# Optimization experiments

Measured on AMD Instinct MI355X. Metric: run time of the kernel, lower is better.

## Reference

```python
import jax, jax.numpy as jnp
import numpy as np

K = 20      # knn fan-in (constructor arg)
EPS = 1e-5  # LayerNorm eps (torch default)

def ln(x, g, b):
    m = jnp.mean(x, axis=-1, keepdims=True)
    v = jnp.mean((x - m) ** 2, axis=-1, keepdims=True)
    return (x - m) / jnp.sqrt(v + EPS) * g + b

def setup_inputs():
    key = jax.random.key(0)
    ks = jax.random.split(key, 12)
    N, Cin, Cout, H = 4096, 128, 128, 512
    def w(k, i, o):
        return (jax.random.normal(k, (i, o), jnp.float32) / np.sqrt(i)).astype(jnp.float32)
    return dict(
        x=jax.random.normal(ks[0], (N, Cin), jnp.float32),
        pos=jax.random.normal(ks[1], (N, 3), jnp.float32),
        batch=jnp.zeros((N,), jnp.int32),
        # PointTransformerConv linears (bias=False in PyG)
        W_lin=w(ks[2], Cin, Cout),
        W_src=w(ks[3], Cin, Cout),
        W_dst=w(ks[4], Cin, Cout),
        # pos_nn: Lin(3,H) LN ELU Lin(H,Cout) LN ELU
        pw1=w(ks[5], 3, H), pb1=jnp.zeros((H,), jnp.float32),
        pg1=jnp.ones((H,), jnp.float32), pbt1=jnp.zeros((H,), jnp.float32),
        pw2=w(ks[6], H, Cout), pb2=jnp.zeros((Cout,), jnp.float32),
        pg2=jnp.ones((Cout,), jnp.float32), pbt2=jnp.zeros((Cout,), jnp.float32),
        # attn_nn: Lin(Cout,H) LN ELU Lin(H,Cout) LN ELU
        aw1=w(ks[7], Cout, H), ab1=jnp.zeros((H,), jnp.float32),
        ag1=jnp.ones((H,), jnp.float32), abt1=jnp.zeros((H,), jnp.float32),
        aw2=w(ks[8], H, Cout), ab2=jnp.zeros((Cout,), jnp.float32),
        ag2=jnp.ones((Cout,), jnp.float32), abt2=jnp.zeros((Cout,), jnp.float32),
    )

def knn_idx(pos):
    # single-graph knn (batch is constant zero); returns [N, K+1] neighbor idx
    # with self-loop appended (PointTransformerConv add_self_loops=True).
    N = pos.shape[0]
    sq = jnp.sum(pos * pos, axis=1)
    d2 = sq[:, None] + sq[None, :] - 2.0 * (pos @ pos.T)      # [N, N]
    d2 = d2.at[jnp.arange(N), jnp.arange(N)].set(jnp.inf)      # loop=False
    _, nbr = jax.lax.top_k(-d2, K)                             # [N, K]
    return jnp.concatenate([nbr, jnp.arange(N)[:, None]], axis=1)

def reference(x, pos, batch, W_lin, W_src, W_dst,
              pw1, pb1, pg1, pbt1, pw2, pb2, pg2, pbt2,
              aw1, ab1, ag1, abt1, aw2, ab2, ag2, abt2):
    idx = knn_idx(pos)                      # [N, K+1] source node per edge
    v = x @ W_lin                           # message values
    a_src = x @ W_src
    a_dst = x @ W_dst
    rel = pos[:, None, :] - pos[idx]        # pos_i - pos_j, [N, K+1, 3]
    h = jax.nn.elu(ln(rel @ pw1 + pb1, pg1, pbt1))
    delta = jax.nn.elu(ln(h @ pw2 + pb2, pg2, pbt2))           # [N, K+1, C]
    alpha = a_dst[:, None, :] - a_src[idx] + delta
    h2 = jax.nn.elu(ln(alpha @ aw1 + ab1, ag1, abt1))
    alpha = jax.nn.elu(ln(h2 @ aw2 + ab2, ag2, abt2))
    alpha = jax.nn.softmax(alpha, axis=1)   # softmax over neighbors of i
    return jnp.sum(alpha * (v[idx] + delta), axis=1)           # [N, C]
```

## Files before the change

### kernel.cpp

```cpp
#include <hip/hip_runtime.h>
#include <math.h>

#define NN    4096
#define CIN   128
#define CO    128
#define HD    512
#define KK    20
#define EE    21
#define EDGES (NN * EE)
#define LNEPS 1e-5f

typedef unsigned short u16;
typedef unsigned int   u32;
typedef unsigned long long u64;
typedef __attribute__((ext_vector_type(8))) short bf16x8;
typedef __attribute__((ext_vector_type(8))) short short8v;
typedef __attribute__((ext_vector_type(4))) float f32x4;

#define MFMA16(a,b,c) __builtin_amdgcn_mfma_f32_16x16x32_bf16(a,b,c,0,0,0)

__device__ __forceinline__ u16 f2b(float x) {
    u32 u = __float_as_uint(x);
    u32 r = u + 0x7fffu + ((u >> 16) & 1u);
    return (u16)(r >> 16);
}
__device__ __forceinline__ float b2f(u16 h) {
    return __uint_as_float(((u32)h) << 16);
}

__global__ __launch_bounds__(64) void k_knn(const float* __restrict__ pos,
                                            int* __restrict__ idxg)
{
    int i = blockIdx.x;
    int lane = threadIdx.x;
    float px = pos[3*i], py = pos[3*i+1], pz = pos[3*i+2];
    float bd[KK]; int bi[KK];
#pragma unroll
    for (int s = 0; s < KK; ++s) { bd[s] = INFINITY; bi[s] = 0x7fffffff; }
    for (int j = lane; j < NN; j += 64) {
        float dx = px - pos[3*j], dy = py - pos[3*j+1], dz = pz - pos[3*j+2];
        float d2 = dx*dx + dy*dy + dz*dz;
        if (j != i && d2 < bd[KK-1]) {
            float cd = d2; int ci = j;
#pragma unroll
            for (int s = 0; s < KK; ++s) {
                bool sw = cd < bd[s];
                float td = sw ? bd[s] : cd;  int ti = sw ? bi[s] : ci;
                bd[s] = sw ? cd : bd[s];     bi[s] = sw ? ci : bi[s];
                cd = td; ci = ti;
            }
        }
    }
    for (int r = 0; r < KK; ++r) {
        u64 m = ~0ull;
#pragma unroll
        for (int s = 0; s < KK; ++s) {
            u64 k = ((u64)__float_as_uint(bd[s]) << 32) | (u32)bi[s];
            m = k < m ? k : m;
        }
#pragma unroll
        for (int off = 32; off > 0; off >>= 1) {
            u64 o = __shfl_xor(m, off, 64);
            m = o < m ? o : m;
        }
        if (lane == 0) idxg[i*EE + r] = (int)(u32)m;
#pragma unroll
        for (int s = 0; s < KK; ++s) {
            u64 k = ((u64)__float_as_uint(bd[s]) << 32) | (u32)bi[s];
            if (k == m) bd[s] = INFINITY;
        }
    }
    if (lane == 0) idxg[i*EE + KK] = i;
}

__global__ __launch_bounds__(256) void k_lin3(const float* __restrict__ x,
        const float* __restrict__ Wl, const float* __restrict__ Ws, const float* __restrict__ Wd,
        float* __restrict__ v, float* __restrict__ as_, float* __restrict__ ad)
{
    __shared__ float sx[8][CIN];
    int b = blockIdx.x, t = threadIdx.x;
    int n0 = b * 8;
    for (int q = t; q < 8*CIN; q += 256) sx[q >> 7][q & 127] = x[n0*CIN + q];
    __syncthreads();
    int c = t & 127, g = t >> 7;
    float al[4] = {0,0,0,0}, asr[4] = {0,0,0,0}, adr[4] = {0,0,0,0};
    for (int k = 0; k < CIN; ++k) {
        float wl = Wl[k*CO + c], ws = Ws[k*CO + c], wd = Wd[k*CO + c];
#pragma unroll
        for (int nn2 = 0; nn2 < 4; ++nn2) {
            float xv = sx[g*4 + nn2][k];
            al[nn2]  = fmaf(xv, wl, al[nn2]);
            asr[nn2] = fmaf(xv, ws, asr[nn2]);
            adr[nn2] = fmaf(xv, wd, adr[nn2]);
        }
    }
#pragma unroll
    for (int nn2 = 0; nn2 < 4; ++nn2) {
        int n = n0 + g*4 + nn2;
        v[n*CO + c]   = al[nn2];
        as_[n*CO + c] = asr[nn2];
        ad[n*CO + c]  = adr[nn2];
    }
}

__global__ __launch_bounds__(256) void k_wconv3(
        const float* __restrict__ aw1, const float* __restrict__ aw2,
        const float* __restrict__ pw2,
        u16* __restrict__ awp1, u16* __restrict__ awp2, u16* __restrict__ pwp2)
{
    int gb = blockIdx.x;
    const float* src; u16* dst; int N, kplog, base;
    if (gb < 256)      { src = aw1; dst = awp1; N = HD; kplog = 2; base = 0;   }
    else if (gb < 512) { src = aw2; dst = awp2; N = CO; kplog = 4; base = 256; }
    else               { src = pw2; dst = pwp2; N = CO; kplog = 4; base = 512; }
    int idx = (gb - base)*256 + threadIdx.x;
    int j  = idx & 7;
    int l  = (idx >> 3) & 63;
    int ks = (idx >> 9) & ((1 << kplog) - 1);
    int nt = idx >> (9 + kplog);
    int k = ks*32 + (l >> 4)*8 + j;
    int c = nt*16 + (l & 15);
    dst[idx] = f2b(src[(size_t)k*N + c]);
}

template<int L>
__device__ __forceinline__ void ln_elu_b16(u16* base, int rows, int stride,
        const float* __restrict__ gam, const float* __restrict__ bet)
{
    constexpr int P = L / 64;
    int t = threadIdx.x, lane = t & 63, w = t >> 6;
    float g[P], b[P];
    if constexpr (P >= 4) {
#pragma unroll
        for (int q = 0; q < P; q += 4) {
            *(float4*)&g[q] = *(const float4*)&gam[lane*P + q];
            *(float4*)&b[q] = *(const float4*)&bet[lane*P + q];
        }
    } else {
        *(float2*)&g[0] = *(const float2*)&gam[lane*P];
        *(float2*)&b[0] = *(const float2*)&bet[lane*P];
    }
    for (int e = w; e < rows; e += 4) {
        u16* row = base + e*stride + lane*P;
        u16 raw[P];
        if constexpr (P == 8) {
            *(ushort4*)&raw[0] = *(const ushort4*)&row[0];
            *(ushort4*)&raw[4] = *(const ushort4*)&row[4];
        } else {
            *(ushort2*)&raw[0] = *(const ushort2*)&row[0];
        }
        float vals[P]; float s = 0.f, sq = 0.f;
#pragma unroll
        for (int q = 0; q < P; ++q) {
            float xx = b2f(raw[q]);
            vals[q] = xx; s += xx; sq += xx*xx;
        }
#pragma unroll
        for (int off = 32; off > 0; off >>= 1) {
            s  += __shfl_xor(s,  off, 64);
            sq += __shfl_xor(sq, off, 64);
        }
        float mn = s * (1.0f / L);
        float rstd = rsqrtf(sq * (1.0f / L) - mn*mn + LNEPS);
#pragma unroll
        for (int q = 0; q < P; ++q) {
            float y = (vals[q] - mn) * rstd * g[q] + b[q];
            y = y > 0.f ? y : __expf(y) - 1.f;
            raw[q] = f2b(y);
        }
        if constexpr (P == 8) {
            *(ushort4*)&row[0] = *(const ushort4*)&raw[0];
            *(ushort4*)&row[4] = *(const ushort4*)&raw[4];
        } else {
            *(ushort2*)&row[0] = *(const ushort2*)&raw[0];
        }
    }
}

#define SA_S 136
#define SH_S 520

__global__ __launch_bounds__(256, 3) void k_posnn(
        const float* __restrict__ pos, const int* __restrict__ idxg,
        const float* __restrict__ pw1, const float* __restrict__ pb1,
        const float* __restrict__ pg1, const float* __restrict__ pbt1,
        const u16* __restrict__ pwp2, const float* __restrict__ pb2,
        const float* __restrict__ pg2, const float* __restrict__ pbt2,
        u16* __restrict__ delta)
{
    __shared__ __align__(16) u16 s_h[32*SH_S];
    __shared__ __align__(16) u16 s_d[32*SA_S];
    __shared__ float s_rel[32][3];
    int t = threadIdx.x;
    int e0g = blockIdx.x * 32;
    if (t < 32) {
        int e = e0g + t;
        u32 ii = (u32)e / 21u;
        int j = idxg[e];
        s_rel[t][0] = pos[3*ii]   - pos[3*j];
        s_rel[t][1] = pos[3*ii+1] - pos[3*j+1];
        s_rel[t][2] = pos[3*ii+2] - pos[3*j+2];
    }
    __syncthreads();
    {
        int c1 = t, c2 = t + 256;
        float wa0 = pw1[c1], wa1 = pw1[HD + c1], wa2 = pw1[2*HD + c1], ba = pb1[c1];
        float wb0 = pw1[c2], wb1 = pw1[HD + c2], wb2 = pw1[2*HD + c2], bb = pb1[c2];
        for (int r = 0; r < 32; ++r) {
            float r0 = s_rel[r][0], r1 = s_rel[r][1], r2 = s_rel[r][2];
            s_h[r*SH_S + c1] = f2b(ba + r0*wa0 + r1*wa1 + r2*wa2);
            s_h[r*SH_S + c2] = f2b(bb + r0*wb0 + r1*wb1 + r2*wb2);
        }
    }
    __syncthreads();
    ln_elu_b16<HD>(s_h, 32, SH_S, pg1, pbt1);
    __syncthreads();
    {
        int w = t >> 6, l = t & 63, lr = l & 15, lk = l >> 4;
        int m = w & 1, nt0 = (w >> 1) * 4;
        bf16x8 afr[16];
#pragma unroll
        for (int ks = 0; ks < 16; ++ks)
            afr[ks] = *(const bf16x8*)&s_h[(m*16 + lr)*SH_S + ks*32 + lk*8];
#pragma unroll
        for (int n2 = 0; n2 < 4; ++n2) {
            int nt = nt0 + n2;
            const u16* bp = pwp2 + ((size_t)nt*16*64 + l)*8;
            f32x4 acc = {0.f, 0.f, 0.f, 0.f};
#pragma unroll
            for (int ks = 0; ks < 16; ++ks) {
                bf16x8 bfr = *(const bf16x8*)(bp + ks*512);
                acc = MFMA16(afr[ks], bfr, acc);
            }
            float bias = pb2[nt*16 + lr];
#pragma unroll
            for (int r = 0; r < 4; ++r)
                s_d[(m*16 + lk*4 + r)*SA_S + nt*16 + lr] = f2b(acc[r] + bias);
        }
    }
    __syncthreads();
    ln_elu_b16<CO>(s_d, 32, SA_S, pg2, pbt2);
    __syncthreads();
    {
        int el = t >> 3, c0 = (t & 7) << 4;
        size_t gb = (size_t)(e0g + el)*CO + c0;
        *(short8v*)&delta[gb]     = *(const short8v*)&s_d[el*SA_S + c0];
        *(short8v*)&delta[gb + 8] = *(const short8v*)&s_d[el*SA_S + c0 + 8];
    }
}

__global__ __launch_bounds__(256, 3) void k_amlp(
        const int* __restrict__ idxg,
        const float* __restrict__ as_, const float* __restrict__ ad,
        const u16* __restrict__ delta,
        const u16* __restrict__ awp1, const float* __restrict__ ab1,
        const float* __restrict__ ag1, const float* __restrict__ abt1,
        const u16* __restrict__ awp2, const float* __restrict__ ab2,
        const float* __restrict__ ag2, const float* __restrict__ abt2,
        u16* __restrict__ alphaF)
{
    __shared__ __align__(16) u16 s_a[32*SA_S];
    __shared__ __align__(16) u16 s_h[32*SH_S];
    __shared__ __align__(16) u16 s_af[32*SA_S];
    int t = threadIdx.x;
    int e0g = blockIdx.x * 32;
    {
        int el = t >> 3, c0 = (t & 7) << 4;
        int e = e0g + el;
        int i = (int)((u32)e / 21u);
        int j = idxg[e];
        const float* adp = ad  + i*CIN + c0;
        const float* asp = as_ + j*CIN + c0;
        const u16*  dp   = delta + (size_t)e*CO + c0;
        u16* op = &s_a[el*SA_S + c0];
#pragma unroll
        for (int q = 0; q < 16; q += 8) {
            float4 a0 = *(const float4*)(adp + q);
            float4 a1 = *(const float4*)(adp + q + 4);
            float4 s0 = *(const float4*)(asp + q);
            float4 s1 = *(const float4*)(asp + q + 4);
            short8v d8 = *(const short8v*)(dp + q);
            short8v o;
            o[0] = (short)f2b(a0.x - s0.x + b2f((u16)d8[0]));
            o[1] = (short)f2b(a0.y - s0.y + b2f((u16)d8[1]));
            o[2] = (short)f2b(a0.z - s0.z + b2f((u16)d8[2]));
            o[3] = (short)f2b(a0.w - s0.w + b2f((u16)d8[3]));
            o[4] = (short)f2b(a1.x - s1.x + b2f((u16)d8[4]));
            o[5] = (short)f2b(a1.y - s1.y + b2f((u16)d8[5]));
            o[6] = (short)f2b(a1.z - s1.z + b2f((u16)d8[6]));
            o[7] = (short)f2b(a1.w - s1.w + b2f((u16)d8[7]));
            *(short8v*)(op + q) = o;
        }
    }
    __syncthreads();
    int w = t >> 6, l = t & 63, lr = l & 15, lk = l >> 4;
    {
        int m = w & 1, nt0 = (w >> 1) * 16;
        bf16x8 afr[4];
#pragma unroll
        for (int ks = 0; ks < 4; ++ks)
            afr[ks] = *(const bf16x8*)&s_a[(m*16 + lr)*SA_S + ks*32 + lk*8];
#pragma unroll
        for (int n2 = 0; n2 < 16; ++n2) {
            int nt = nt0 + n2;
            const u16* bp = awp1 + ((size_t)nt*4*64 + l)*8;
            f32x4 acc = {0.f, 0.f, 0.f, 0.f};
#pragma unroll
            for (int ks = 0; ks < 4; ++ks) {
                bf16x8 bfr = *(const bf16x8*)(bp + ks*512);
                acc = MFMA16(afr[ks], bfr, acc);
            }
            float bias = ab1[nt*16 + lr];
#pragma unroll
            for (int r = 0; r < 4; ++r)
                s_h[(m*16 + lk*4 + r)*SH_S + nt*16 + lr] = f2b(acc[r] + bias);
        }
    }
    __syncthreads();
    ln_elu_b16<HD>(s_h, 32, SH_S, ag1, abt1);
    __syncthreads();
    {
        int m = w & 1, nt0 = (w >> 1) * 4;
        bf16x8 afr[16];
#pragma unroll
        for (int ks = 0; ks < 16; ++ks)
            afr[ks] = *(const bf16x8*)&s_h[(m*16 + lr)*SH_S + ks*32 + lk*8];
#pragma unroll
        for (int n2 = 0; n2 < 4; ++n2) {
            int nt = nt0 + n2;
            const u16* bp = awp2 + ((size_t)nt*16*64 + l)*8;
            f32x4 acc = {0.f, 0.f, 0.f, 0.f};
#pragma unroll
            for (int ks = 0; ks < 16; ++ks) {
                bf16x8 bfr = *(const bf16x8*)(bp + ks*512);
                acc = MFMA16(afr[ks], bfr, acc);
            }
            float bias = ab2[nt*16 + lr];
#pragma unroll
            for (int r = 0; r < 4; ++r)
                s_af[(m*16 + lk*4 + r)*SA_S + nt*16 + lr] = f2b(acc[r] + bias);
        }
    }
    __syncthreads();
    ln_elu_b16<CO>(s_af, 32, SA_S, ag2, abt2);
    __syncthreads();
    {
        int el = t >> 3, c0 = (t & 7) << 4;
        size_t gb = (size_t)(e0g + el)*CO + c0;
        *(short8v*)&alphaF[gb]     = *(const short8v*)&s_af[el*SA_S + c0];
        *(short8v*)&alphaF[gb + 8] = *(const short8v*)&s_af[el*SA_S + c0 + 8];
    }
}

__global__ __launch_bounds__(256) void k_agg(
        const int* __restrict__ idxg,
        const float* __restrict__ v, const u16* __restrict__ delta,
        const u16* __restrict__ alphaF, float* __restrict__ out)
{
    __shared__ int s_idx[8][EE];
    int b = blockIdx.x, t = threadIdx.x;
    int n0 = b * 8;
    for (int q = t; q < 8*EE; q += 256) s_idx[q/EE][q%EE] = idxg[n0*EE + q];
    __syncthreads();
    int c = t & 127, g = t >> 7;
    for (int ng = g; ng < 8; ng += 2) {
        int i = n0 + ng;
        size_t base = (size_t)i*EE*CO + c;
        float af[EE]; float mx = -INFINITY;
#pragma unroll
        for (int e = 0; e < EE; ++e) { af[e] = b2f(alphaF[base + e*CO]); mx = fmaxf(mx, af[e]); }
        float ssum = 0.f;
#pragma unroll
        for (int e = 0; e < EE; ++e) { af[e] = __expf(af[e] - mx); ssum += af[e]; }
        float accv = 0.f;
#pragma unroll
        for (int e = 0; e < EE; ++e) {
            int j = s_idx[ng][e];
            float msg = v[j*CO + c] + b2f(delta[base + e*CO]);
            accv = fmaf(af[e], msg, accv);
        }
        out[i*CO + c] = accv / ssum;
    }
}

extern "C" void kernel_launch(void* const* d_in, const int* in_sizes, int n_in,
                              void* d_out, int out_size, void* d_ws, size_t ws_size,
                              hipStream_t stream)
{
    const float* x    = (const float*)d_in[0];
    const float* pos  = (const float*)d_in[1];
    const float* Wl   = (const float*)d_in[3];
    const float* Wsrc = (const float*)d_in[4];
    const float* Wdst = (const float*)d_in[5];
    const float* pw1  = (const float*)d_in[6];
    const float* pb1  = (const float*)d_in[7];
    const float* pg1  = (const float*)d_in[8];
    const float* pbt1 = (const float*)d_in[9];
    const float* pw2  = (const float*)d_in[10];
    const float* pb2  = (const float*)d_in[11];
    const float* pg2  = (const float*)d_in[12];
    const float* pbt2 = (const float*)d_in[13];
    const float* aw1  = (const float*)d_in[14];
    const float* ab1  = (const float*)d_in[15];
    const float* ag1  = (const float*)d_in[16];
    const float* abt1 = (const float*)d_in[17];
    const float* aw2  = (const float*)d_in[18];
    const float* ab2  = (const float*)d_in[19];
    const float* ag2  = (const float*)d_in[20];
    const float* abt2 = (const float*)d_in[21];
    float* out = (float*)d_out;

    char* ws = (char*)d_ws;
    int*   idxg   = (int*)ws;
    u16*   awp1   = (u16*)(ws + 0x54000);
    u16*   awp2   = (u16*)(ws + 0x74000);
    u16*   pwp2   = (u16*)(ws + 0x94000);
    float* v      = (float*)(ws + 0xC0000);
    float* asrc   = (float*)(ws + 0x2C0000);
    float* adst   = (float*)(ws + 0x4C0000);
    u16*   delta  = (u16*)(ws + 0x6C0000);
    u16*   alphaF = (u16*)(ws + 0x6C0000 + 0x1500000);

    k_knn   <<<NN,       64,  0, stream>>>(pos, idxg);
    k_wconv3<<<768,      256, 0, stream>>>(aw1, aw2, pw2, awp1, awp2, pwp2);
    k_lin3  <<<NN/8,     256, 0, stream>>>(x, Wl, Wsrc, Wdst, v, asrc, adst);
    k_posnn <<<EDGES/32, 256, 0, stream>>>(pos, idxg, pw1, pb1, pg1, pbt1,
                                           pwp2, pb2, pg2, pbt2, delta);
    k_amlp  <<<EDGES/32, 256, 0, stream>>>(idxg, asrc, adst, delta,
                                           awp1, ab1, ag1, abt1,
                                           awp2, ab2, ag2, abt2, alphaF);
    k_agg   <<<NN/8,     256, 0, stream>>>(idxg, v, delta, alphaF, out);
}
```

Before: 301.8 us.

## Double block size to 512 threads in edge MLP kernels, keep second GEMM output in fp32

The posnn and attention-MLP kernels now launch 512 threads (8 waves) per 32-edge tile, so each wave computes half as many MFMA output tiles and LayerNorm rows. The second linear's output is kept in fp32 in shared memory, skipping a bf16 round trip before the final LayerNorm, and is converted to bf16 only on the global store. This adds parallelism per tile but raises shared memory use and drops the occupancy hint of 3 blocks, so occupancy may change.

```diff
diff --git a/kernel.cpp b/kernel.cpp
--- a/kernel.cpp
+++ b/kernel.cpp
@@ -14,7 +14,6 @@
 typedef unsigned int   u32;
 typedef unsigned long long u64;
 typedef __attribute__((ext_vector_type(8))) short bf16x8;
-typedef __attribute__((ext_vector_type(8))) short short8v;
 typedef __attribute__((ext_vector_type(4))) float f32x4;
 
 #define MFMA16(a,b,c) __builtin_amdgcn_mfma_f32_16x16x32_bf16(a,b,c,0,0,0)
@@ -123,32 +122,23 @@
     dst[idx] = f2b(src[(size_t)k*N + c]);
 }
 
-template<int L>
+template<int L, int NW>
 __device__ __forceinline__ void ln_elu_b16(u16* base, int rows, int stride,
         const float* __restrict__ gam, const float* __restrict__ bet)
 {
     constexpr int P = L / 64;
     int t = threadIdx.x, lane = t & 63, w = t >> 6;
     float g[P], b[P];
-    if constexpr (P >= 4) {
-#pragma unroll
-        for (int q = 0; q < P; q += 4) {
-            *(float4*)&g[q] = *(const float4*)&gam[lane*P + q];
-            *(float4*)&b[q] = *(const float4*)&bet[lane*P + q];
-        }
-    } else {
-        *(float2*)&g[0] = *(const float2*)&gam[lane*P];
-        *(float2*)&b[0] = *(const float2*)&bet[lane*P];
-    }
-    for (int e = w; e < rows; e += 4) {
+#pragma unroll
+    for (int q = 0; q < P; q += 4) {
+        *(float4*)&g[q] = *(const float4*)&gam[lane*P + q];
+        *(float4*)&b[q] = *(const float4*)&bet[lane*P + q];
+    }
+    for (int e = w; e < rows; e += NW) {
         u16* row = base + e*stride + lane*P;
         u16 raw[P];
-        if constexpr (P == 8) {
-            *(ushort4*)&raw[0] = *(const ushort4*)&row[0];
-            *(ushort4*)&raw[4] = *(const ushort4*)&row[4];
-        } else {
-            *(ushort2*)&raw[0] = *(const ushort2*)&row[0];
-        }
+        *(ushort4*)&raw[0] = *(const ushort4*)&row[0];
+        *(ushort4*)&raw[4] = *(const ushort4*)&row[4];
         float vals[P]; float s = 0.f, sq = 0.f;
 #pragma unroll
         for (int q = 0; q < P; ++q) {
@@ -168,19 +158,48 @@
             y = y > 0.f ? y : __expf(y) - 1.f;
             raw[q] = f2b(y);
         }
-        if constexpr (P == 8) {
-            *(ushort4*)&row[0] = *(const ushort4*)&raw[0];
-            *(ushort4*)&row[4] = *(const ushort4*)&raw[4];
-        } else {
-            *(ushort2*)&row[0] = *(const ushort2*)&raw[0];
-        }
+        *(ushort4*)&row[0] = *(const ushort4*)&raw[0];
+        *(ushort4*)&row[4] = *(const ushort4*)&raw[4];
+    }
+}
+
+template<int L, int NW>
+__device__ __forceinline__ void ln_elu_f32v(float* base, int rows, int stride,
+        const float* __restrict__ gam, const float* __restrict__ bet)
+{
+    constexpr int P = L / 64;
+    int t = threadIdx.x, lane = t & 63, w = t >> 6;
+    float g[P], b[P];
+    *(float2*)&g[0] = *(const float2*)&gam[lane*P];
+    *(float2*)&b[0] = *(const float2*)&bet[lane*P];
+    for (int e = w; e < rows; e += NW) {
+        float* row = base + e*stride + lane*P;
+        float vals[P];
+        *(float2*)&vals[0] = *(const float2*)&row[0];
+        float s = 0.f, sq = 0.f;
+#pragma unroll
+        for (int q = 0; q < P; ++q) { s += vals[q]; sq += vals[q]*vals[q]; }
+#pragma unroll
+        for (int off = 32; off > 0; off >>= 1) {
+            s  += __shfl_xor(s,  off, 64);
+            sq += __shfl_xor(sq, off, 64);
+        }
+        float mn = s * (1.0f / L);
+        float rstd = rsqrtf(sq * (1.0f / L) - mn*mn + LNEPS);
+#pragma unroll
+        for (int q = 0; q < P; ++q) {
+            float y = (vals[q] - mn) * rstd * g[q] + b[q];
+            vals[q] = y > 0.f ? y : __expf(y) - 1.f;
+        }
+        *(float2*)&row[0] = *(const float2*)&vals[0];
     }
 }
 
 #define SA_S 136
 #define SH_S 520
-
-__global__ __launch_bounds__(256, 3) void k_posnn(
+#define SF_S 132
+
+__global__ __launch_bounds__(512) void k_posnn(
         const float* __restrict__ pos, const int* __restrict__ idxg,
         const float* __restrict__ pw1, const float* __restrict__ pb1,
         const float* __restrict__ pg1, const float* __restrict__ pbt1,
@@ -188,8 +207,8 @@
         const float* __restrict__ pg2, const float* __restrict__ pbt2,
         u16* __restrict__ delta)
 {
-    __shared__ __align__(16) u16 s_h[32*SH_S];
-    __shared__ __align__(16) u16 s_d[32*SA_S];
+    __shared__ __align__(16) u16   s_h[32*SH_S];
+    __shared__ __align__(16) float s_d[32*SF_S];
     __shared__ float s_rel[32][3];
     int t = threadIdx.x;
     int e0g = blockIdx.x * 32;
@@ -203,27 +222,25 @@
     }
     __syncthreads();
     {
-        int c1 = t, c2 = t + 256;
+        int c1 = t;
         float wa0 = pw1[c1], wa1 = pw1[HD + c1], wa2 = pw1[2*HD + c1], ba = pb1[c1];
-        float wb0 = pw1[c2], wb1 = pw1[HD + c2], wb2 = pw1[2*HD + c2], bb = pb1[c2];
         for (int r = 0; r < 32; ++r) {
-            float r0 = s_rel[r][0], r1 = s_rel[r][1], r2 = s_rel[r][2];
-            s_h[r*SH_S + c1] = f2b(ba + r0*wa0 + r1*wa1 + r2*wa2);
-            s_h[r*SH_S + c2] = f2b(bb + r0*wb0 + r1*wb1 + r2*wb2);
-        }
-    }
-    __syncthreads();
-    ln_elu_b16<HD>(s_h, 32, SH_S, pg1, pbt1);
+            float hv = fmaf(s_rel[r][2], wa2, fmaf(s_rel[r][1], wa1, fmaf(s_rel[r][0], wa0, ba)));
+            s_h[r*SH_S + c1] = f2b(hv);
+        }
+    }
+    __syncthreads();
+    ln_elu_b16<HD, 8>(s_h, 32, SH_S, pg1, pbt1);
     __syncthreads();
     {
         int w = t >> 6, l = t & 63, lr = l & 15, lk = l >> 4;
-        int m = w & 1, nt0 = (w >> 1) * 4;
+        int m = w & 1, nt0 = (w >> 1) * 2;
         bf16x8 afr[16];
 #pragma unroll
         for (int ks = 0; ks < 16; ++ks)
             afr[ks] = *(const bf16x8*)&s_h[(m*16 + lr)*SH_S + ks*32 + lk*8];
 #pragma unroll
-        for (int n2 = 0; n2 < 4; ++n2) {
+        for (int n2 = 0; n2 < 2; ++n2) {
             int nt = nt0 + n2;
             const u16* bp = pwp2 + ((size_t)nt*16*64 + l)*8;
             f32x4 acc = {0.f, 0.f, 0.f, 0.f};
@@ -235,21 +252,27 @@
             float bias = pb2[nt*16 + lr];
 #pragma unroll
             for (int r = 0; r < 4; ++r)
-                s_d[(m*16 + lk*4 + r)*SA_S + nt*16 + lr] = f2b(acc[r] + bias);
-        }
-    }
-    __syncthreads();
-    ln_elu_b16<CO>(s_d, 32, SA_S, pg2, pbt2);
-    __syncthreads();
-    {
-        int el = t >> 3, c0 = (t & 7) << 4;
-        size_t gb = (size_t)(e0g + el)*CO + c0;
-        *(short8v*)&delta[gb]     = *(const short8v*)&s_d[el*SA_S + c0];
-        *(short8v*)&delta[gb + 8] = *(const short8v*)&s_d[el*SA_S + c0 + 8];
-    }
-}
-
-__global__ __launch_bounds__(256, 3) void k_amlp(
+                s_d[(m*16 + lk*4 + r)*SF_S + nt*16 + lr] = acc[r] + bias;
+        }
+    }
+    __syncthreads();
+    ln_elu_f32v<CO, 8>(s_d, 32, SF_S, pg2, pbt2);
+    __syncthreads();
+    {
+        int el = t >> 4, c0 = (t & 15) << 3;
+        const float* sp = &s_d[el*SF_S + c0];
+        float4 v0 = *(const float4*)(sp);
+        float4 v1 = *(const float4*)(sp + 4);
+        bf16x8 o;
+        o[0] = (short)f2b(v0.x); o[1] = (short)f2b(v0.y);
+        o[2] = (short)f2b(v0.z); o[3] = (short)f2b(v0.w);
+        o[4] = (short)f2b(v1.x); o[5] = (short)f2b(v1.y);
+        o[6] = (short)f2b(v1.z); o[7] = (short)f2b(v1.w);
+        *(bf16x8*)&delta[(size_t)(e0g + el)*CO + c0] = o;
+    }
+}
+
+__global__ __launch_bounds__(512) void k_amlp(
         const int* __restrict__ idxg,
         const float* __restrict__ as_, const float* __restrict__ ad,
         const u16* __restrict__ delta,
@@ -259,49 +282,45 @@
         const float* __restrict__ ag2, const float* __restrict__ abt2,
         u16* __restrict__ alphaF)
 {
-    __shared__ __align__(16) u16 s_a[32*SA_S];
-    __shared__ __align__(16) u16 s_h[32*SH_S];
-    __shared__ __align__(16) u16 s_af[32*SA_S];
+    __shared__ __align__(16) u16   s_a[32*SA_S];
+    __shared__ __align__(16) u16   s_h[32*SH_S];
+    __shared__ __align__(16) float s_af[32*SF_S];
     int t = threadIdx.x;
     int e0g = blockIdx.x * 32;
     {
-        int el = t >> 3, c0 = (t & 7) << 4;
+        int el = t >> 4, c0 = (t & 15) << 3;
         int e = e0g + el;
         int i = (int)((u32)e / 21u);
         int j = idxg[e];
         const float* adp = ad  + i*CIN + c0;
         const float* asp = as_ + j*CIN + c0;
         const u16*  dp   = delta + (size_t)e*CO + c0;
-        u16* op = &s_a[el*SA_S + c0];
-#pragma unroll
-        for (int q = 0; q < 16; q += 8) {
-            float4 a0 = *(const float4*)(adp + q);
-            float4 a1 = *(const float4*)(adp + q + 4);
-            float4 s0 = *(const float4*)(asp + q);
-            float4 s1 = *(const float4*)(asp + q + 4);
-            short8v d8 = *(const short8v*)(dp + q);
-            short8v o;
-            o[0] = (short)f2b(a0.x - s0.x + b2f((u16)d8[0]));
-            o[1] = (short)f2b(a0.y - s0.y + b2f((u16)d8[1]));
-            o[2] = (short)f2b(a0.z - s0.z + b2f((u16)d8[2]));
-            o[3] = (short)f2b(a0.w - s0.w + b2f((u16)d8[3]));
-            o[4] = (short)f2b(a1.x - s1.x + b2f((u16)d8[4]));
-            o[5] = (short)f2b(a1.y - s1.y + b2f((u16)d8[5]));
-            o[6] = (short)f2b(a1.z - s1.z + b2f((u16)d8[6]));
-            o[7] = (short)f2b(a1.w - s1.w + b2f((u16)d8[7]));
-            *(short8v*)(op + q) = o;
-        }
+        float4 a0 = *(const float4*)(adp);
+        float4 a1 = *(const float4*)(adp + 4);
+        float4 s0 = *(const float4*)(asp);
+        float4 s1 = *(const float4*)(asp + 4);
+        bf16x8 d8 = *(const bf16x8*)(dp);
+        bf16x8 o;
+        o[0] = (short)f2b(a0.x - s0.x + b2f((u16)d8[0]));
+        o[1] = (short)f2b(a0.y - s0.y + b2f((u16)d8[1]));
+        o[2] = (short)f2b(a0.z - s0.z + b2f((u16)d8[2]));
+        o[3] = (short)f2b(a0.w - s0.w + b2f((u16)d8[3]));
+        o[4] = (short)f2b(a1.x - s1.x + b2f((u16)d8[4]));
+        o[5] = (short)f2b(a1.y - s1.y + b2f((u16)d8[5]));
+        o[6] = (short)f2b(a1.z - s1.z + b2f((u16)d8[6]));
+        o[7] = (short)f2b(a1.w - s1.w + b2f((u16)d8[7]));
+        *(bf16x8*)&s_a[el*SA_S + c0] = o;
     }
     __syncthreads();
     int w = t >> 6, l = t & 63, lr = l & 15, lk = l >> 4;
     {
-        int m = w & 1, nt0 = (w >> 1) * 16;
+        int m = w & 1, nt0 = (w >> 1) * 8;
         bf16x8 afr[4];
 #pragma unroll
         for (int ks = 0; ks < 4; ++ks)
             afr[ks] = *(const bf16x8*)&s_a[(m*16 + lr)*SA_S + ks*32 + lk*8];
 #pragma unroll
-        for (int n2 = 0; n2 < 16; ++n2) {
+        for (int n2 = 0; n2 < 8; ++n2) {
             int nt = nt0 + n2;
             const u16* bp = awp1 + ((size_t)nt*4*64 + l)*8;
             f32x4 acc = {0.f, 0.f, 0.f, 0.f};
@@ -317,16 +336,16 @@
         }
     }
     __syncthreads();
-    ln_elu_b16<HD>(s_h, 32, SH_S, ag1, abt1);
-    __syncthreads();
-    {
-        int m = w & 1, nt0 = (w >> 1) * 4;
+    ln_elu_b16<HD, 8>(s_h, 32, SH_S, ag1, abt1);
+    __syncthreads();
+    {
+        int m = w & 1, nt0 = (w >> 1) * 2;
         bf16x8 afr[16];
 #pragma unroll
         for (int ks = 0; ks < 16; ++ks)
             afr[ks] = *(const bf16x8*)&s_h[(m*16 + lr)*SH_S + ks*32 + lk*8];
 #pragma unroll
-        for (int n2 = 0; n2 < 4; ++n2) {
+        for (int n2 = 0; n2 < 2; ++n2) {
             int nt = nt0 + n2;
             const u16* bp = awp2 + ((size_t)nt*16*64 + l)*8;
             f32x4 acc = {0.f, 0.f, 0.f, 0.f};
@@ -338,17 +357,23 @@
             float bias = ab2[nt*16 + lr];
 #pragma unroll
             for (int r = 0; r < 4; ++r)
-                s_af[(m*16 + lk*4 + r)*SA_S + nt*16 + lr] = f2b(acc[r] + bias);
-        }
-    }
-    __syncthreads();
-    ln_elu_b16<CO>(s_af, 32, SA_S, ag2, abt2);
-    __syncthreads();
-    {
-        int el = t >> 3, c0 = (t & 7) << 4;
-        size_t gb = (size_t)(e0g + el)*CO + c0;
-        *(short8v*)&alphaF[gb]     = *(const short8v*)&s_af[el*SA_S + c0];
-        *(short8v*)&alphaF[gb + 8] = *(const short8v*)&s_af[el*SA_S + c0 + 8];
+                s_af[(m*16 + lk*4 + r)*SF_S + nt*16 + lr] = acc[r] + bias;
+        }
+    }
+    __syncthreads();
+    ln_elu_f32v<CO, 8>(s_af, 32, SF_S, ag2, abt2);
+    __syncthreads();
+    {
+        int el = t >> 4, c0 = (t & 15) << 3;
+        const float* sp = &s_af[el*SF_S + c0];
+        float4 v0 = *(const float4*)(sp);
+        float4 v1 = *(const float4*)(sp + 4);
+        bf16x8 o;
+        o[0] = (short)f2b(v0.x); o[1] = (short)f2b(v0.y);
+        o[2] = (short)f2b(v0.z); o[3] = (short)f2b(v0.w);
+        o[4] = (short)f2b(v1.x); o[5] = (short)f2b(v1.y);
+        o[6] = (short)f2b(v1.z); o[7] = (short)f2b(v1.w);
+        *(bf16x8*)&alphaF[(size_t)(e0g + el)*CO + c0] = o;
     }
 }
 
@@ -424,9 +449,9 @@
     k_knn   <<<NN,       64,  0, stream>>>(pos, idxg);
     k_wconv3<<<768,      256, 0, stream>>>(aw1, aw2, pw2, awp1, awp2, pwp2);
     k_lin3  <<<NN/8,     256, 0, stream>>>(x, Wl, Wsrc, Wdst, v, asrc, adst);
-    k_posnn <<<EDGES/32, 256, 0, stream>>>(pos, idxg, pw1, pb1, pg1, pbt1,
+    k_posnn <<<EDGES/32, 512, 0, stream>>>(pos, idxg, pw1, pb1, pg1, pbt1,
                                            pwp2, pb2, pg2, pbt2, delta);
-    k_amlp  <<<EDGES/32, 256, 0, stream>>>(idxg, asrc, adst, delta,
+    k_amlp  <<<EDGES/32, 512, 0, stream>>>(idxg, asrc, adst, delta,
                                            awp1, ab1, ag1, abt1,
                                            awp2, ab2, ag2, abt2, alphaF);
     k_agg   <<<NN/8,     256, 0, stream>>>(idxg, v, delta, alphaF, out);
```

Measured after the change: 292.0 us. -3.2%, faster.
